# Performance work log

Measured on AMD Instinct MI355X. Metric: run time of the kernel, lower is better.

Reference implementation:

```python
import jax, jax.numpy as jnp
import numpy as np

B, V, F, P, E = 4, 8192, 16384, 4, 2048


def setup_inputs() -> dict:
    key = jax.random.key(0)
    k1, k2, k3, k4, k5 = jax.random.split(key, 5)
    xs = jax.random.normal(k1, (B, V, 3), dtype=jnp.float32)
    y = jax.random.normal(k2, (B, V, 3), dtype=jnp.float32)
    # projection matrices [P,3,4]; make the 3rd (homogeneous-divide) row
    # close to [0,0,0,1] so projected depth ~1 and the divide is stable.
    pm = jax.random.normal(k3, (P, 3, 4), dtype=jnp.float32)
    pm = pm.at[:, 2, :].set(jnp.asarray([0.0, 0.0, 0.0, 1.0], jnp.float32)
                            + 0.01 * jax.random.normal(k5, (P, 4), dtype=jnp.float32))
    edgemaps = jax.random.normal(k4, (B, P, E, 2), dtype=jnp.float32)
    faces = jax.random.randint(jax.random.fold_in(key, 7), (B, F, 3), 0, V, dtype=jnp.int32)
    return {"xs": xs, "y": y, "projmatrices": pm, "edgemaps": edgemaps, "faces": faces}


def _volumes(verts, faces):
    fv = jax.vmap(lambda v, f: v[f])(verts, faces)        # [B,F,3,3]
    v0, v1, v2 = fv[:, :, 0], fv[:, :, 1], fv[:, :, 2]
    face_vol = jnp.sum(jnp.cross(v0, v1) * v2, axis=-1) / 6.0  # [B,F]
    return jnp.abs(jnp.sum(face_vol, axis=-1))                 # [B]


def reference(xs, y, projmatrices, edgemaps, faces):
    lambda_proj, lambda_vol = 1.0, 1.0
    # ---- lsq_proj: per-mesh SSE between original and projected verts ----
    lsq = jnp.sum(jnp.square(xs - y), axis=(-1, -2))            # [B]
    # ---- volume constraint (target volume is a fixed buffer from src) ----
    target_vol = jax.lax.stop_gradient(_volumes(xs, faces))
    vol_loss = jnp.square(_volumes(y, faces) - target_vol)      # [B]
    # ---- silhouette chamfer: project verts into P views, chamfer vs edgemaps
    ones = jnp.ones((B, V, 1), dtype=y.dtype)
    y_h = jnp.concatenate([y, ones], axis=-1)                   # [B,V,4]
    proj = jnp.einsum('pij,bvj->bpvi', projmatrices, y_h)       # [B,P,V,3]
    pts = proj[..., :2] / proj[..., 2:3]                        # [B,P,V,2]
    # pairwise squared distances [B,P,V,E]
    d2 = jnp.sum(jnp.square(pts[:, :, :, None, :] - edgemaps[:, :, None, :, :]), axis=-1)
    cham_x = jnp.mean(jnp.min(d2, axis=3), axis=2)              # [B,P] boundary->edgemap
    cham_y = jnp.mean(jnp.min(d2, axis=2), axis=2)              # [B,P] edgemap->boundary
    chamfer = jnp.mean(cham_x + cham_y, axis=1)                 # [B] batch_reduction='mean' over views
    return chamfer + lambda_proj * lsq + lambda_vol * vol_loss
```

## Files before the change

### kernel.cpp

```cpp
#include <hip/hip_runtime.h>

#define B 4
#define V 8192
#define F 16384
#define P 4
#define E 2048
#define NPAIR (B*P)

#define WS_PTS   0
#define WS_ER    524288
#define WS_VMIN  655360
#define WS_EMIN  786432
#define WS_CX    819200
#define WS_CY    819216
#define WS_VOLX  819232
#define WS_VOLY  819236
#define WS_LSQ   819240

#define INFBITS 0x7F800000u

__device__ __forceinline__ float block_sum(float v, float* sred) {
    #pragma unroll
    for (int off = 32; off; off >>= 1) v += __shfl_down(v, off, 64);
    int w = threadIdx.x >> 6, l = threadIdx.x & 63;
    if (l == 0) sred[w] = v;
    __syncthreads();
    float r = 0.f;
    if (threadIdx.x == 0) {
        r = sred[0];
        for (int i = 1; i < ((int)blockDim.x >> 6); ++i) r += sred[i];
    }
    __syncthreads();
    return r;
}

__global__ void __launch_bounds__(256) k_init(const float* __restrict__ em,
                                              float* __restrict__ ws) {
    int i = blockIdx.x * 256 + threadIdx.x;
    ((unsigned*)(ws + WS_VMIN))[i] = INFBITS;
    if (i < NPAIR * E) {
        ((unsigned*)(ws + WS_EMIN))[i] = INFBITS;
        float2 e = ((const float2*)em)[i];
        ((float4*)(ws + WS_ER))[i] = make_float4(e.x, e.y, e.x * e.x + e.y * e.y, 0.f);
    }
    if (i < 44) ws[WS_CX + i] = 0.f;
}

__global__ void __launch_bounds__(256) k_proj(const float* __restrict__ xs,
                                              const float* __restrict__ y,
                                              const float* __restrict__ pm,
                                              float* __restrict__ ws) {
    __shared__ float spm[48];
    __shared__ float sred[4];
    int tid = threadIdx.x;
    if (tid < 48) spm[tid] = pm[tid];
    __syncthreads();
    int b = blockIdx.x >> 5;
    int v = ((blockIdx.x & 31) << 8) + tid;
    size_t base = ((size_t)b * V + v) * 3;
    float y0 = y[base], y1 = y[base + 1], y2 = y[base + 2];
    float x0 = xs[base], x1 = xs[base + 1], x2 = xs[base + 2];
    float d0 = x0 - y0, d1 = x1 - y1, d2 = x2 - y2;
    float lsq = d0 * d0 + d1 * d1 + d2 * d2;

    float4* pts = (float4*)(ws + WS_PTS);
    #pragma unroll
    for (int p = 0; p < P; ++p) {
        const float* m = spm + p * 12;
        float xw = m[0] * y0 + m[1] * y1 + m[2]  * y2 + m[3];
        float yw = m[4] * y0 + m[5] * y1 + m[6]  * y2 + m[7];
        float w  = m[8] * y0 + m[9] * y1 + m[10] * y2 + m[11];
        float px = xw / w, py = yw / w;
        pts[(size_t)(b * P + p) * V + v] = make_float4(px, py, px * px + py * py, 0.f);
    }

    float s = block_sum(lsq, sred);
    if (tid == 0) atomicAdd(ws + WS_LSQ + b, s);
}

__device__ __forceinline__ float facevol(const float* __restrict__ vb,
                                         int i0, int i1, int i2) {
    float a0 = vb[i0 * 3], a1 = vb[i0 * 3 + 1], a2 = vb[i0 * 3 + 2];
    float b0 = vb[i1 * 3], b1 = vb[i1 * 3 + 1], b2 = vb[i1 * 3 + 2];
    float c0 = vb[i2 * 3], c1 = vb[i2 * 3 + 1], c2 = vb[i2 * 3 + 2];
    float cx = a1 * b2 - a2 * b1;
    float cy = a2 * b0 - a0 * b2;
    float cz = a0 * b1 - a1 * b0;
    return (cx * c0 + cy * c1 + cz * c2) * (1.0f / 6.0f);
}

__global__ void __launch_bounds__(256) k_vol(const float* __restrict__ xs,
                                             const float* __restrict__ y,
                                             const int* __restrict__ faces,
                                             float* __restrict__ ws) {
    __shared__ float sred[4];
    int tid = threadIdx.x;
    int b = blockIdx.x >> 6;
    int f = ((blockIdx.x & 63) << 8) + tid;
    size_t fb = ((size_t)b * F + f) * 3;
    int i0 = faces[fb], i1 = faces[fb + 1], i2 = faces[fb + 2];
    const float* xb = xs + (size_t)b * V * 3;
    const float* yb = y  + (size_t)b * V * 3;
    float fvx = facevol(xb, i0, i1, i2);
    float fvy = facevol(yb, i0, i1, i2);
    float sx = block_sum(fvx, sred);
    float sy = block_sum(fvy, sred);
    if (tid == 0) {
        atomicAdd(ws + WS_VOLX + b, sx);
        atomicAdd(ws + WS_VOLY + b, sy);
    }
}

__global__ void __launch_bounds__(256) k_chamx(float* __restrict__ ws) {
    __shared__ float4 se[256];
    int tid = threadIdx.x;
    int blk = blockIdx.x;
    int pair = blk >> 5;
    int vch = (blk >> 3) & 3;
    int ech = blk & 7;

    se[tid] = ((const float4*)(ws + WS_ER))[(size_t)pair * E + ech * 256 + tid];

    const float4* pts = (const float4*)(ws + WS_PTS) + (size_t)pair * V + vch * 2048 + tid;
    float px2[8], py2[8], pz[8], mn[8];
    #pragma unroll
    for (int k = 0; k < 8; ++k) {
        float4 p = pts[k * 256];
        px2[k] = -2.f * p.x; py2[k] = -2.f * p.y; pz[k] = p.z;
        mn[k] = 3.4e38f;
    }
    __syncthreads();

    #pragma unroll 4
    for (int i = 0; i < 256; ++i) {
        float4 e = se[i];
        #pragma unroll
        for (int k = 0; k < 8; ++k)
            mn[k] = fminf(mn[k], fmaf(px2[k], e.x, fmaf(py2[k], e.y, e.z)));
    }

    unsigned* vmin = (unsigned*)(ws + WS_VMIN) + (size_t)pair * V + vch * 2048 + tid;
    #pragma unroll
    for (int k = 0; k < 8; ++k)
        atomicMin(vmin + k * 256, __float_as_uint(mn[k] + pz[k]));
}

__global__ void __launch_bounds__(256) k_chamy(float* __restrict__ ws) {
    __shared__ float4 sp[256];
    int tid = threadIdx.x;
    int blk = blockIdx.x;
    int pair = blk >> 5;
    int vch = blk & 31;

    sp[tid] = ((const float4*)(ws + WS_PTS))[(size_t)pair * V + vch * 256 + tid];

    const float4* er = (const float4*)(ws + WS_ER) + (size_t)pair * E + tid;
    float ex2[8], ey2[8], ez[8], mn[8];
    #pragma unroll
    for (int k = 0; k < 8; ++k) {
        float4 e = er[k * 256];
        ex2[k] = -2.f * e.x; ey2[k] = -2.f * e.y; ez[k] = e.z;
        mn[k] = 3.4e38f;
    }
    __syncthreads();

    #pragma unroll 4
    for (int i = 0; i < 256; ++i) {
        float4 p = sp[i];
        #pragma unroll
        for (int k = 0; k < 8; ++k)
            mn[k] = fminf(mn[k], fmaf(ex2[k], p.x, fmaf(ey2[k], p.y, p.z)));
    }

    unsigned* emin = (unsigned*)(ws + WS_EMIN) + (size_t)pair * E + tid;
    #pragma unroll
    for (int k = 0; k < 8; ++k)
        atomicMin(emin + k * 256, __float_as_uint(mn[k] + ez[k]));
}

__global__ void __launch_bounds__(256) k_red(float* __restrict__ ws) {
    __shared__ float sred[4];
    int tid = threadIdx.x;
    int blk = blockIdx.x;
    float val;
    float* dst;
    if (blk < 512) {
        int idx = blk * 256 + tid;
        val = ws[WS_VMIN + idx] * (1.0f / V);
        dst = ws + WS_CX + (blk >> 5);
    } else {
        int idx = (blk - 512) * 256 + tid;
        val = ws[WS_EMIN + idx] * (1.0f / E);
        dst = ws + WS_CY + ((blk - 512) >> 3);
    }
    float s = block_sum(val, sred);
    if (tid == 0) atomicAdd(dst, s);
}

__global__ void k_out(float* __restrict__ ws, float* __restrict__ out) {
    int b = threadIdx.x;
    if (b < B) {
        float c = 0.f;
        for (int p = 0; p < P; ++p) {
            int pair = b * P + p;
            c += ws[WS_CX + pair] + ws[WS_CY + pair];
        }
        c *= (1.0f / P);
        float vx = fabsf(ws[WS_VOLX + b]);
        float vy = fabsf(ws[WS_VOLY + b]);
        float dv = vy - vx;
        out[b] = c + ws[WS_LSQ + b] + dv * dv;
    }
}

extern "C" void kernel_launch(void* const* d_in, const int* in_sizes, int n_in,
                              void* d_out, int out_size, void* d_ws, size_t ws_size,
                              hipStream_t stream) {
    const float* xs    = (const float*)d_in[0];
    const float* y     = (const float*)d_in[1];
    const float* pm    = (const float*)d_in[2];
    const float* em    = (const float*)d_in[3];
    const int*   faces = (const int*)d_in[4];
    float* ws  = (float*)d_ws;
    float* out = (float*)d_out;

    hipLaunchKernelGGL(k_init,  dim3(512),         dim3(256), 0, stream, em, ws);
    hipLaunchKernelGGL(k_proj,  dim3(B * V / 256), dim3(256), 0, stream, xs, y, pm, ws);
    hipLaunchKernelGGL(k_vol,   dim3(B * F / 256), dim3(256), 0, stream, xs, y, faces, ws);
    hipLaunchKernelGGL(k_chamx, dim3(512),         dim3(256), 0, stream, ws);
    hipLaunchKernelGGL(k_chamy, dim3(512),         dim3(256), 0, stream, ws);
    hipLaunchKernelGGL(k_red,   dim3(640),         dim3(256), 0, stream, ws);
    hipLaunchKernelGGL(k_out,   dim3(1),           dim3(64),  0, stream, ws, out);
}
```

Measured before the change: 123.8 us.

## Merge seven launches into three kernels and drop atomic partial-sum accumulation

Combines the init, projection and volume kernels into a single block-partitioned preprocessing kernel, and merges both chamfer directions into one launch. Per-block partial sums are now written to distinct slots instead of being accumulated atomically, so no zeroing is needed. A 4-block final kernel performs the min-array reduction and the output combine. This reduces launch overhead and inter-kernel gaps, but the final reduction now runs on only 4 blocks, which may serialize work that was previously spread over 640 blocks.

After: 136.9 us. 1.11x slower.

```diff
diff --git a/kernel.cpp b/kernel.cpp
--- a/kernel.cpp
+++ b/kernel.cpp
@@ -5,17 +5,15 @@
 #define F 16384
 #define P 4
 #define E 2048
-#define NPAIR (B*P)
+#define NPAIR 16
 
 #define WS_PTS   0
 #define WS_ER    524288
 #define WS_VMIN  655360
 #define WS_EMIN  786432
-#define WS_CX    819200
-#define WS_CY    819216
-#define WS_VOLX  819232
-#define WS_VOLY  819236
-#define WS_LSQ   819240
+#define WS_LSQP  819200
+#define WS_VOLPX 819328
+#define WS_VOLPY 819584
 
 #define INFBITS 0x7F800000u
 
@@ -34,50 +32,6 @@
     return r;
 }
 
-__global__ void __launch_bounds__(256) k_init(const float* __restrict__ em,
-                                              float* __restrict__ ws) {
-    int i = blockIdx.x * 256 + threadIdx.x;
-    ((unsigned*)(ws + WS_VMIN))[i] = INFBITS;
-    if (i < NPAIR * E) {
-        ((unsigned*)(ws + WS_EMIN))[i] = INFBITS;
-        float2 e = ((const float2*)em)[i];
-        ((float4*)(ws + WS_ER))[i] = make_float4(e.x, e.y, e.x * e.x + e.y * e.y, 0.f);
-    }
-    if (i < 44) ws[WS_CX + i] = 0.f;
-}
-
-__global__ void __launch_bounds__(256) k_proj(const float* __restrict__ xs,
-                                              const float* __restrict__ y,
-                                              const float* __restrict__ pm,
-                                              float* __restrict__ ws) {
-    __shared__ float spm[48];
-    __shared__ float sred[4];
-    int tid = threadIdx.x;
-    if (tid < 48) spm[tid] = pm[tid];
-    __syncthreads();
-    int b = blockIdx.x >> 5;
-    int v = ((blockIdx.x & 31) << 8) + tid;
-    size_t base = ((size_t)b * V + v) * 3;
-    float y0 = y[base], y1 = y[base + 1], y2 = y[base + 2];
-    float x0 = xs[base], x1 = xs[base + 1], x2 = xs[base + 2];
-    float d0 = x0 - y0, d1 = x1 - y1, d2 = x2 - y2;
-    float lsq = d0 * d0 + d1 * d1 + d2 * d2;
-
-    float4* pts = (float4*)(ws + WS_PTS);
-    #pragma unroll
-    for (int p = 0; p < P; ++p) {
-        const float* m = spm + p * 12;
-        float xw = m[0] * y0 + m[1] * y1 + m[2]  * y2 + m[3];
-        float yw = m[4] * y0 + m[5] * y1 + m[6]  * y2 + m[7];
-        float w  = m[8] * y0 + m[9] * y1 + m[10] * y2 + m[11];
-        float px = xw / w, py = yw / w;
-        pts[(size_t)(b * P + p) * V + v] = make_float4(px, py, px * px + py * py, 0.f);
-    }
-
-    float s = block_sum(lsq, sred);
-    if (tid == 0) atomicAdd(ws + WS_LSQ + b, s);
-}
-
 __device__ __forceinline__ float facevol(const float* __restrict__ vb,
                                          int i0, int i1, int i2) {
     float a0 = vb[i0 * 3], a1 = vb[i0 * 3 + 1], a2 = vb[i0 * 3 + 2];
@@ -89,127 +43,145 @@
     return (cx * c0 + cy * c1 + cz * c2) * (1.0f / 6.0f);
 }
 
-__global__ void __launch_bounds__(256) k_vol(const float* __restrict__ xs,
+__global__ void __launch_bounds__(256) k_pre(const float* __restrict__ xs,
                                              const float* __restrict__ y,
+                                             const float* __restrict__ pm,
+                                             const float* __restrict__ em,
                                              const int* __restrict__ faces,
                                              float* __restrict__ ws) {
-    __shared__ float sred[4];
-    int tid = threadIdx.x;
-    int b = blockIdx.x >> 6;
-    int f = ((blockIdx.x & 63) << 8) + tid;
-    size_t fb = ((size_t)b * F + f) * 3;
-    int i0 = faces[fb], i1 = faces[fb + 1], i2 = faces[fb + 2];
-    const float* xb = xs + (size_t)b * V * 3;
-    const float* yb = y  + (size_t)b * V * 3;
-    float fvx = facevol(xb, i0, i1, i2);
-    float fvy = facevol(yb, i0, i1, i2);
-    float sx = block_sum(fvx, sred);
-    float sy = block_sum(fvy, sred);
-    if (tid == 0) {
-        atomicAdd(ws + WS_VOLX + b, sx);
-        atomicAdd(ws + WS_VOLY + b, sy);
-    }
-}
-
-__global__ void __launch_bounds__(256) k_chamx(float* __restrict__ ws) {
-    __shared__ float4 se[256];
-    int tid = threadIdx.x;
-    int blk = blockIdx.x;
-    int pair = blk >> 5;
-    int vch = (blk >> 3) & 3;
-    int ech = blk & 7;
-
-    se[tid] = ((const float4*)(ws + WS_ER))[(size_t)pair * E + ech * 256 + tid];
-
-    const float4* pts = (const float4*)(ws + WS_PTS) + (size_t)pair * V + vch * 2048 + tid;
-    float px2[8], py2[8], pz[8], mn[8];
-    #pragma unroll
-    for (int k = 0; k < 8; ++k) {
-        float4 p = pts[k * 256];
-        px2[k] = -2.f * p.x; py2[k] = -2.f * p.y; pz[k] = p.z;
-        mn[k] = 3.4e38f;
-    }
-    __syncthreads();
-
-    #pragma unroll 4
-    for (int i = 0; i < 256; ++i) {
-        float4 e = se[i];
-        #pragma unroll
-        for (int k = 0; k < 8; ++k)
-            mn[k] = fminf(mn[k], fmaf(px2[k], e.x, fmaf(py2[k], e.y, e.z)));
-    }
-
-    unsigned* vmin = (unsigned*)(ws + WS_VMIN) + (size_t)pair * V + vch * 2048 + tid;
-    #pragma unroll
-    for (int k = 0; k < 8; ++k)
-        atomicMin(vmin + k * 256, __float_as_uint(mn[k] + pz[k]));
-}
-
-__global__ void __launch_bounds__(256) k_chamy(float* __restrict__ ws) {
-    __shared__ float4 sp[256];
-    int tid = threadIdx.x;
-    int blk = blockIdx.x;
-    int pair = blk >> 5;
-    int vch = blk & 31;
-
-    sp[tid] = ((const float4*)(ws + WS_PTS))[(size_t)pair * V + vch * 256 + tid];
-
-    const float4* er = (const float4*)(ws + WS_ER) + (size_t)pair * E + tid;
-    float ex2[8], ey2[8], ez[8], mn[8];
-    #pragma unroll
-    for (int k = 0; k < 8; ++k) {
-        float4 e = er[k * 256];
-        ex2[k] = -2.f * e.x; ey2[k] = -2.f * e.y; ez[k] = e.z;
-        mn[k] = 3.4e38f;
-    }
-    __syncthreads();
-
-    #pragma unroll 4
-    for (int i = 0; i < 256; ++i) {
-        float4 p = sp[i];
-        #pragma unroll
-        for (int k = 0; k < 8; ++k)
-            mn[k] = fminf(mn[k], fmaf(ex2[k], p.x, fmaf(ey2[k], p.y, p.z)));
-    }
-
-    unsigned* emin = (unsigned*)(ws + WS_EMIN) + (size_t)pair * E + tid;
-    #pragma unroll
-    for (int k = 0; k < 8; ++k)
-        atomicMin(emin + k * 256, __float_as_uint(mn[k] + ez[k]));
-}
-
-__global__ void __launch_bounds__(256) k_red(float* __restrict__ ws) {
+    __shared__ float spm[48];
     __shared__ float sred[4];
     int tid = threadIdx.x;
     int blk = blockIdx.x;
-    float val;
-    float* dst;
+
+    if (blk < 128) {
+        if (tid < 48) spm[tid] = pm[tid];
+        __syncthreads();
+        int b = blk >> 5;
+        int v = ((blk & 31) << 8) + tid;
+        size_t base = ((size_t)b * V + v) * 3;
+        float y0 = y[base], y1 = y[base + 1], y2 = y[base + 2];
+        float x0 = xs[base], x1 = xs[base + 1], x2 = xs[base + 2];
+        float d0 = x0 - y0, d1 = x1 - y1, d2 = x2 - y2;
+        float lsq = d0 * d0 + d1 * d1 + d2 * d2;
+
+        float4* pts = (float4*)(ws + WS_PTS);
+        #pragma unroll
+        for (int p = 0; p < P; ++p) {
+            const float* m = spm + p * 12;
+            float xw = m[0] * y0 + m[1] * y1 + m[2]  * y2 + m[3];
+            float yw = m[4] * y0 + m[5] * y1 + m[6]  * y2 + m[7];
+            float w  = m[8] * y0 + m[9] * y1 + m[10] * y2 + m[11];
+            float px = xw / w, py = yw / w;
+            pts[(size_t)(b * P + p) * V + v] = make_float4(px, py, px * px + py * py, 0.f);
+        }
+        float s = block_sum(lsq, sred);
+        if (tid == 0) ws[WS_LSQP + blk] = s;
+    } else if (blk < 384) {
+        int blk2 = blk - 128;
+        int b = blk2 >> 6;
+        int f = ((blk2 & 63) << 8) + tid;
+        size_t fb = ((size_t)b * F + f) * 3;
+        int i0 = faces[fb], i1 = faces[fb + 1], i2 = faces[fb + 2];
+        const float* xb = xs + (size_t)b * V * 3;
+        const float* yb = y  + (size_t)b * V * 3;
+        float sx = block_sum(facevol(xb, i0, i1, i2), sred);
+        float sy = block_sum(facevol(yb, i0, i1, i2), sred);
+        if (tid == 0) { ws[WS_VOLPX + blk2] = sx; ws[WS_VOLPY + blk2] = sy; }
+    } else {
+        int i = (blk - 384) * 256 + tid;
+        ((unsigned*)(ws + WS_VMIN))[i] = INFBITS;
+        if (i < NPAIR * E) {
+            ((unsigned*)(ws + WS_EMIN))[i] = INFBITS;
+            float2 e = ((const float2*)em)[i];
+            ((float4*)(ws + WS_ER))[i] = make_float4(e.x, e.y, e.x * e.x + e.y * e.y, 0.f);
+        }
+    }
+}
+
+__global__ void __launch_bounds__(256) k_cham(float* __restrict__ ws) {
+    __shared__ float4 sbuf[256];
+    int tid = threadIdx.x;
+    int blk = blockIdx.x;
+
     if (blk < 512) {
-        int idx = blk * 256 + tid;
-        val = ws[WS_VMIN + idx] * (1.0f / V);
-        dst = ws + WS_CX + (blk >> 5);
+        int pair = blk >> 5;
+        int vch = (blk >> 3) & 3;
+        int ech = blk & 7;
+        sbuf[tid] = ((const float4*)(ws + WS_ER))[(size_t)pair * E + ech * 256 + tid];
+
+        const float4* pts = (const float4*)(ws + WS_PTS) + (size_t)pair * V + vch * 2048 + tid;
+        float px2[8], py2[8], pz[8], mn[8];
+        #pragma unroll
+        for (int k = 0; k < 8; ++k) {
+            float4 p = pts[k * 256];
+            px2[k] = -2.f * p.x; py2[k] = -2.f * p.y; pz[k] = p.z;
+            mn[k] = 3.4e38f;
+        }
+        __syncthreads();
+        #pragma unroll 4
+        for (int i = 0; i < 256; ++i) {
+            float4 e = sbuf[i];
+            #pragma unroll
+            for (int k = 0; k < 8; ++k)
+                mn[k] = fminf(mn[k], fmaf(px2[k], e.x, fmaf(py2[k], e.y, e.z)));
+        }
+        unsigned* vmin = (unsigned*)(ws + WS_VMIN) + (size_t)pair * V + vch * 2048 + tid;
+        #pragma unroll
+        for (int k = 0; k < 8; ++k)
+            atomicMin(vmin + k * 256, __float_as_uint(mn[k] + pz[k]));
     } else {
-        int idx = (blk - 512) * 256 + tid;
-        val = ws[WS_EMIN + idx] * (1.0f / E);
-        dst = ws + WS_CY + ((blk - 512) >> 3);
-    }
-    float s = block_sum(val, sred);
-    if (tid == 0) atomicAdd(dst, s);
-}
-
-__global__ void k_out(float* __restrict__ ws, float* __restrict__ out) {
-    int b = threadIdx.x;
-    if (b < B) {
-        float c = 0.f;
-        for (int p = 0; p < P; ++p) {
-            int pair = b * P + p;
-            c += ws[WS_CX + pair] + ws[WS_CY + pair];
-        }
-        c *= (1.0f / P);
-        float vx = fabsf(ws[WS_VOLX + b]);
-        float vy = fabsf(ws[WS_VOLY + b]);
-        float dv = vy - vx;
-        out[b] = c + ws[WS_LSQ + b] + dv * dv;
+        int blk2 = blk - 512;
+        int pair = blk2 >> 5;
+        int vch = blk2 & 31;
+        sbuf[tid] = ((const float4*)(ws + WS_PTS))[(size_t)pair * V + vch * 256 + tid];
+
+        const float4* er = (const float4*)(ws + WS_ER) + (size_t)pair * E + tid;
+        float ex2[8], ey2[8], ez[8], mn[8];
+        #pragma unroll
+        for (int k = 0; k < 8; ++k) {
+            float4 e = er[k * 256];
+            ex2[k] = -2.f * e.x; ey2[k] = -2.f * e.y; ez[k] = e.z;
+            mn[k] = 3.4e38f;
+        }
+        __syncthreads();
+        #pragma unroll 4
+        for (int i = 0; i < 256; ++i) {
+            float4 p = sbuf[i];
+            #pragma unroll
+            for (int k = 0; k < 8; ++k)
+                mn[k] = fminf(mn[k], fmaf(ex2[k], p.x, fmaf(ey2[k], p.y, p.z)));
+        }
+        unsigned* emin = (unsigned*)(ws + WS_EMIN) + (size_t)pair * E + tid;
+        #pragma unroll
+        for (int k = 0; k < 8; ++k)
+            atomicMin(emin + k * 256, __float_as_uint(mn[k] + ez[k]));
+    }
+}
+
+__global__ void __launch_bounds__(256) k_fin(float* __restrict__ ws,
+                                             float* __restrict__ out) {
+    __shared__ float sred[4];
+    int tid = threadIdx.x;
+    int b = blockIdx.x;
+    const float* vmin = ws + WS_VMIN;
+    const float* emin = ws + WS_EMIN;
+
+    float sv = 0.f, se = 0.f;
+    #pragma unroll
+    for (int p = 0; p < P; ++p) {
+        size_t vb = (size_t)(b * P + p) * V;
+        for (int i = tid; i < V; i += 256) sv += vmin[vb + i];
+        size_t eb = (size_t)(b * P + p) * E;
+        for (int i = tid; i < E; i += 256) se += emin[eb + i];
+    }
+    float cham = block_sum(sv * (1.0f / (V * P)) + se * (1.0f / (E * P)), sred);
+    float volx = block_sum((tid < 64) ? ws[WS_VOLPX + b * 64 + tid] : 0.f, sred);
+    float voly = block_sum((tid < 64) ? ws[WS_VOLPY + b * 64 + tid] : 0.f, sred);
+    float lsq  = block_sum((tid < 32) ? ws[WS_LSQP  + b * 32 + tid] : 0.f, sred);
+    if (tid == 0) {
+        float dv = fabsf(voly) - fabsf(volx);
+        out[b] = cham + lsq + dv * dv;
     }
 }
 
@@ -224,11 +196,7 @@
     float* ws  = (float*)d_ws;
     float* out = (float*)d_out;
 
-    hipLaunchKernelGGL(k_init,  dim3(512),         dim3(256), 0, stream, em, ws);
-    hipLaunchKernelGGL(k_proj,  dim3(B * V / 256), dim3(256), 0, stream, xs, y, pm, ws);
-    hipLaunchKernelGGL(k_vol,   dim3(B * F / 256), dim3(256), 0, stream, xs, y, faces, ws);
-    hipLaunchKernelGGL(k_chamx, dim3(512),         dim3(256), 0, stream, ws);
-    hipLaunchKernelGGL(k_chamy, dim3(512),         dim3(256), 0, stream, ws);
-    hipLaunchKernelGGL(k_red,   dim3(640),         dim3(256), 0, stream, ws);
-    hipLaunchKernelGGL(k_out,   dim3(1),           dim3(64),  0, stream, ws, out);
-}
+    hipLaunchKernelGGL(k_pre,  dim3(896),  dim3(256), 0, stream, xs, y, pm, em, faces, ws);
+    hipLaunchKernelGGL(k_cham, dim3(1024), dim3(256), 0, stream, ws);
+    hipLaunchKernelGGL(k_fin,  dim3(4),    dim3(256), 0, stream, ws, out);
+}
```
